# Optimization experiments

Hardware: AMD Instinct MI355X
Metric: run time of the kernel (lower is better)

Reference implementation:

```python
import jax, jax.numpy as jnp
import numpy as np

B, S, DIN, DH, NB = 4, 2048, 256, 128, 50
LN_EPS = 1e-5
THRESHOLDS = (0.5, 1.0, 2.0, 4.0)


def _layernorm(x, g, b):
    m = jnp.mean(x, axis=-1, keepdims=True)
    v = jnp.mean((x - m) ** 2, axis=-1, keepdims=True)
    return (x - m) * jax.lax.rsqrt(v + LN_EPS) * g + b


def setup_inputs() -> dict:
    key = jax.random.key(0)
    ks = jax.random.split(key, 12)
    single_repr = jax.random.normal(ks[0], (B, S, DIN), jnp.float32)
    # coordinates spread out so the <=15A local neighborhood is nontrivial
    coordinates = jax.random.normal(ks[1], (B, S, 3), jnp.float32) * 12.0
    mask = jnp.ones((B, S), jnp.float32)
    sc = 0.05
    return {
        'single_repr': single_repr,
        'coordinates': coordinates,
        'mask': mask,
        'W1': jax.random.normal(ks[2], (DIN, DH), jnp.float32) * sc,
        'b1': jnp.zeros((DH,), jnp.float32),
        'g1': jnp.ones((DH,), jnp.float32),
        'be1': jnp.zeros((DH,), jnp.float32),
        'W2': jax.random.normal(ks[3], (DH, DH), jnp.float32) * sc,
        'b2': jnp.zeros((DH,), jnp.float32),
        'g2': jnp.ones((DH,), jnp.float32),
        'be2': jnp.zeros((DH,), jnp.float32),
        'W3': jax.random.normal(ks[4], (DH, NB), jnp.float32) * sc,
        'b3': jnp.zeros((NB,), jnp.float32),
        'temperature': jnp.ones((1,), jnp.float32),
    }


def reference(single_repr, coordinates, mask, W1, b1, g1, be1, W2, b2, g2, be2, W3, b3, temperature):
    # ---- confidence MLP (dropout in eval mode = identity) ----
    h = jax.nn.relu(_layernorm(single_repr @ W1 + b1, g1, be1))
    h = jax.nn.relu(_layernorm(h @ W2 + b2, g2, be2))
    logits = (h @ W3 + b3) / temperature          # [B, S, NB]
    probs = jax.nn.softmax(logits, axis=-1)

    # ---- vectorized pLDDT (replaces the per-residue Python loop) ----
    diff = coordinates[:, :, None, :] - coordinates[:, None, :, :]   # [B,S,S,3]
    D = jnp.sqrt(jnp.sum(diff * diff, axis=-1))                      # [B,S,S]
    maskb = mask > 0.0
    local = (D <= 15.0) & maskb[:, :, None] & maskb[:, None, :]      # [B,S,S]
    counts = jnp.sum(local, axis=-1).astype(jnp.float32)             # [B,S]
    frac_sum = jnp.zeros((B, S), jnp.float32)
    for t in THRESHOLDS:  # fixed small loop over 4 thresholds
        within = jnp.sum((D <= t) & local, axis=-1).astype(jnp.float32)
        frac_sum = frac_sum + within / jnp.maximum(counts, 1.0)
    plddt = jnp.where(counts > 0, frac_sum / len(THRESHOLDS) * 100.0, 0.0)

    # ---- final masking, as in torch forward ----
    plddt = plddt * mask
    logits_m = logits * mask[:, :, None]
    probs_m = probs * mask[:, :, None]
    return plddt, logits_m, probs_m
```

## Files before the change

kernel.cpp:

```cpp
#include <hip/hip_runtime.h>
#include <float.h>
#include <math.h>

#define B_   4
#define S_   2048
#define DIN_ 256
#define DH_  128
#define NB_  50
#define NBP_ 64
#define ROWS (B_ * S_)
#define MB   16

#define MLP_BLOCKS   (ROWS / MB)
#define PLDDT_ROWSPB 32
#define PLDDT_BLOCKS (ROWS / PLDDT_ROWSPB)

typedef __attribute__((ext_vector_type(8))) short  short8;
typedef __attribute__((ext_vector_type(4))) float  f32x4;

__device__ __forceinline__ unsigned short bf16_rne(float f) {
    unsigned u = __builtin_bit_cast(unsigned, f);
    u = u + 0x7fffu + ((u >> 16) & 1u);
    return (unsigned short)(u >> 16);
}

__global__ __launch_bounds__(256) void setup_w(
    const float* __restrict__ W1, const float* __restrict__ W2,
    const float* __restrict__ W3, unsigned short* __restrict__ wt)
{
    const int t = blockIdx.x * 256 + threadIdx.x;
    const int l = t & 63, m = l & 15, kg = l >> 4;
    float src[8];
    int dst;
    if (t < 4096) {
        const int c = t >> 6, nt = c >> 3, ks = c & 7;
        const int n = nt * 16 + m, k = ks * 32 + kg * 8;
#pragma unroll
        for (int i = 0; i < 8; ++i) src[i] = W1[(k + i) * DH_ + n];
        dst = t * 8;
    } else if (t < 6144) {
        const int s = t - 4096, c = s >> 6, nt = c >> 2, ks = c & 3;
        const int n = nt * 16 + m, k = ks * 32 + kg * 8;
#pragma unroll
        for (int i = 0; i < 8; ++i) src[i] = W2[(k + i) * DH_ + n];
        dst = 32768 + s * 8;
    } else {
        const int s = t - 6144, c = s >> 6, nt = c >> 2, ks = c & 3;
        const int n = nt * 16 + m, k = ks * 32 + kg * 8;
#pragma unroll
        for (int i = 0; i < 8; ++i) src[i] = (n < NB_) ? W3[(k + i) * NB_ + n] : 0.f;
        dst = 49152 + s * 8;
    }
    union { short8 v; unsigned short u[8]; } H;
#pragma unroll
    for (int i = 0; i < 8; ++i) H.u[i] = bf16_rne(src[i]);
    *(short8*)&wt[dst] = H.v;
}

union SharedU {
    struct {
        unsigned short sA[MB * DIN_];
        float sStats[MB][20];
        float sL[MB * NBP_];
    } mlp;
    f32x4 sP[S_];
};

__global__ __launch_bounds__(512) void fused_kernel(
    const float* __restrict__ x, const float* __restrict__ coords,
    const float* __restrict__ mask,
    const float* __restrict__ b1, const float* __restrict__ g1, const float* __restrict__ be1,
    const float* __restrict__ b2, const float* __restrict__ g2, const float* __restrict__ be2,
    const float* __restrict__ b3, const float* __restrict__ temp,
    const unsigned short* __restrict__ wt,
    float* __restrict__ out_plddt,
    float* __restrict__ out_logits, float* __restrict__ out_probs)
{
    __shared__ SharedU sh;
    const int tid  = threadIdx.x;
    const int lane = tid & 63;
    const int w    = tid >> 6;

    if (blockIdx.x < MLP_BLOCKS) {
        unsigned short* sA = sh.mlp.sA;
        const int m    = lane & 15;
        const int kg   = lane >> 4;
        const int row0 = blockIdx.x * MB;

        {
            const int r  = tid >> 5;
            const int kc = (tid & 31) << 3;
            const float* xp = x + (size_t)(row0 + r) * DIN_ + kc;
            f32x4 a = *(const f32x4*)xp;
            f32x4 b = *(const f32x4*)(xp + 4);
            union { short8 v; unsigned short u[8]; } H;
#pragma unroll
            for (int i = 0; i < 8; ++i)
                H.u[i] = bf16_rne((i < 4) ? a[i] : b[i - 4]);
            const int idx = (r * 256 + kc) ^ ((r & 7) << 3);
            *(short8*)&sA[idx] = H.v;
        }
        __syncthreads();

        const int n12 = w * 16 + m;

        f32x4 aA = {0.f,0.f,0.f,0.f}, aB = {0.f,0.f,0.f,0.f};
        {
            const unsigned short* bp = wt + (w * 8) * 512;
#pragma unroll
            for (int ks = 0; ks < 8; ++ks) {
                const int ia = (m * 256 + ks * 32 + kg * 8) ^ ((m & 7) << 3);
                short8 ah = *(const short8*)&sA[ia];
                short8 bh = *(const short8*)&bp[ks * 512 + lane * 8];
                f32x4& ac = (ks & 1) ? aB : aA;
                ac = __builtin_amdgcn_mfma_f32_16x16x32_bf16(ah, bh, ac, 0, 0, 0);
            }
        }

        {
            const float bb = b1[n12], gg = g1[n12], ee = be1[n12];
            float v[4];
#pragma unroll
            for (int j = 0; j < 4; ++j) v[j] = aA[j] + aB[j] + bb;
#pragma unroll
            for (int j = 0; j < 4; ++j) {
                float sv = v[j], qv = v[j] * v[j];
                for (int off = 1; off < 16; off <<= 1) { sv += __shfl_xor(sv, off); qv += __shfl_xor(qv, off); }
                if (m == 0) { sh.mlp.sStats[kg * 4 + j][w * 2] = sv; sh.mlp.sStats[kg * 4 + j][w * 2 + 1] = qv; }
            }
            __syncthreads();
#pragma unroll
            for (int j = 0; j < 4; ++j) {
                const int r = kg * 4 + j;
                f32x4 s0 = *(const f32x4*)&sh.mlp.sStats[r][0];
                f32x4 s1 = *(const f32x4*)&sh.mlp.sStats[r][4];
                f32x4 s2 = *(const f32x4*)&sh.mlp.sStats[r][8];
                f32x4 s3 = *(const f32x4*)&sh.mlp.sStats[r][12];
                const float S = s0[0]+s0[2]+s1[0]+s1[2]+s2[0]+s2[2]+s3[0]+s3[2];
                const float Q = s0[1]+s0[3]+s1[1]+s1[3]+s2[1]+s2[3]+s3[1]+s3[3];
                const float mean = S * (1.f / DH_);
                const float inv  = rsqrtf(Q * (1.f / DH_) - mean * mean + 1e-5f);
                const float h = fmaxf(fmaf((v[j] - mean) * inv, gg, ee), 0.f);
                const int idx = (r * 128 + n12) ^ ((r & 7) << 3);
                sA[idx] = bf16_rne(h);
            }
        }
        __syncthreads();

        aA = (f32x4){0.f,0.f,0.f,0.f}; aB = (f32x4){0.f,0.f,0.f,0.f};
        {
            const unsigned short* bp = wt + 32768 + (w * 4) * 512;
#pragma unroll
            for (int ks = 0; ks < 4; ++ks) {
                const int ia = (m * 128 + ks * 32 + kg * 8) ^ ((m & 7) << 3);
                short8 ah = *(const short8*)&sA[ia];
                short8 bh = *(const short8*)&bp[ks * 512 + lane * 8];
                f32x4& ac = (ks & 1) ? aB : aA;
                ac = __builtin_amdgcn_mfma_f32_16x16x32_bf16(ah, bh, ac, 0, 0, 0);
            }
        }

        {
            const float bb = b2[n12], gg = g2[n12], ee = be2[n12];
            float v[4];
#pragma unroll
            for (int j = 0; j < 4; ++j) v[j] = aA[j] + aB[j] + bb;
#pragma unroll
            for (int j = 0; j < 4; ++j) {
                float sv = v[j], qv = v[j] * v[j];
                for (int off = 1; off < 16; off <<= 1) { sv += __shfl_xor(sv, off); qv += __shfl_xor(qv, off); }
                if (m == 0) { sh.mlp.sStats[kg * 4 + j][w * 2] = sv; sh.mlp.sStats[kg * 4 + j][w * 2 + 1] = qv; }
            }
            __syncthreads();
#pragma unroll
            for (int j = 0; j < 4; ++j) {
                const int r = kg * 4 + j;
                f32x4 s0 = *(const f32x4*)&sh.mlp.sStats[r][0];
                f32x4 s1 = *(const f32x4*)&sh.mlp.sStats[r][4];
                f32x4 s2 = *(const f32x4*)&sh.mlp.sStats[r][8];
                f32x4 s3 = *(const f32x4*)&sh.mlp.sStats[r][12];
                const float S = s0[0]+s0[2]+s1[0]+s1[2]+s2[0]+s2[2]+s3[0]+s3[2];
                const float Q = s0[1]+s0[3]+s1[1]+s1[3]+s2[1]+s2[3]+s3[1]+s3[3];
                const float mean = S * (1.f / DH_);
                const float inv  = rsqrtf(Q * (1.f / DH_) - mean * mean + 1e-5f);
                const float h = fmaxf(fmaf((v[j] - mean) * inv, gg, ee), 0.f);
                const int idx = (r * 128 + n12) ^ ((r & 7) << 3);
                sA[idx] = bf16_rne(h);
            }
        }
        __syncthreads();

        if (w < 4) {
            f32x4 cA = {0.f,0.f,0.f,0.f}, cB = {0.f,0.f,0.f,0.f};
            const unsigned short* bp = wt + 49152 + (w * 4) * 512;
#pragma unroll
            for (int ks = 0; ks < 4; ++ks) {
                const int ia = (m * 128 + ks * 32 + kg * 8) ^ ((m & 7) << 3);
                short8 ah = *(const short8*)&sA[ia];
                short8 bh = *(const short8*)&bp[ks * 512 + lane * 8];
                f32x4& ac = (ks & 1) ? cB : cA;
                ac = __builtin_amdgcn_mfma_f32_16x16x32_bf16(ah, bh, ac, 0, 0, 0);
            }
            const int n = w * 16 + m;
            const float bv = (n < NB_) ? b3[n] : 0.f;
            const float invT = 1.f / temp[0];
#pragma unroll
            for (int j = 0; j < 4; ++j)
                sh.mlp.sL[(kg * 4 + j) * NBP_ + n] = (cA[j] + cB[j] + bv) * invT;
        }
        __syncthreads();

        if (tid < 256) {
            const int r  = tid >> 4;
            const int c0 = (tid & 15) * 4;
            f32x4 lg = *(const f32x4*)&sh.mlp.sL[r * NBP_ + c0];
            float mx = -FLT_MAX;
#pragma unroll
            for (int i = 0; i < 4; ++i) if (c0 + i < NB_) mx = fmaxf(mx, lg[i]);
            for (int off = 1; off < 16; off <<= 1) mx = fmaxf(mx, __shfl_xor(mx, off));
            float e[4]; float sm = 0.f;
#pragma unroll
            for (int i = 0; i < 4; ++i) { e[i] = (c0 + i < NB_) ? expf(lg[i] - mx) : 0.f; sm += e[i]; }
            for (int off = 1; off < 16; off <<= 1) sm += __shfl_xor(sm, off);
            const float isum = 1.f / sm;
            const float mk = mask[row0 + r];
            float* ol = out_logits + (size_t)(row0 + r) * NB_;
            float* op = out_probs  + (size_t)(row0 + r) * NB_;
#pragma unroll
            for (int i = 0; i < 4; ++i) {
                const int c = c0 + i;
                if (c < NB_) { ol[c] = lg[i] * mk; op[c] = e[i] * isum * mk; }
            }
        }
    } else {
        const int pb   = blockIdx.x - MLP_BLOCKS;
        const int row0 = pb * PLDDT_ROWSPB;
        const int b    = row0 >> 11;
        const int ib0  = row0 & (S_ - 1);

        const float* cb = coords + (size_t)b * S_ * 3;
        const float* mb = mask   + (size_t)b * S_;

        {
            union { f32x4 v[3]; float f[12]; } C;
            const float* cp = cb + tid * 12;
#pragma unroll
            for (int q = 0; q < 3; ++q) C.v[q] = *(const f32x4*)(cp + q * 4);
            union { f32x4 v; float f[4]; } M;
            M.v = *(const f32x4*)(mb + tid * 4);
#pragma unroll
            for (int q = 0; q < 4; ++q)
                sh.sP[tid * 4 + q] = (f32x4){C.f[q*3], C.f[q*3+1], C.f[q*3+2], M.f[q]};
        }
        __syncthreads();

        f32x4 PI[4];
#pragma unroll
        for (int ii = 0; ii < 4; ++ii) PI[ii] = sh.sP[ib0 + w * 4 + ii];

        int cnt[4] = {0,0,0,0}, wsum[4] = {0,0,0,0};
        for (int j = lane; j < S_; j += 64) {
            const f32x4 p = sh.sP[j];
            const float gd = (p[3] > 0.f) ? 0.f : 1e30f;
#pragma unroll
            for (int ii = 0; ii < 4; ++ii) {
                const float dx = PI[ii][0] - p[0];
                const float dy = PI[ii][1] - p[1];
                const float dz = PI[ii][2] - p[2];
                const float d2 = fmaf(dx, dx, fmaf(dy, dy, dz * dz)) + gd;
                cnt[ii]  += (d2 <= 225.f);
                wsum[ii] += (d2 <= 16.f);
                wsum[ii] += (d2 <= 4.f);
                wsum[ii] += (d2 <= 1.f);
                wsum[ii] += (d2 <= 0.25f);
            }
        }
#pragma unroll
        for (int ii = 0; ii < 4; ++ii)
            for (int off = 32; off; off >>= 1) {
                cnt[ii]  += __shfl_xor(cnt[ii], off);
                wsum[ii] += __shfl_xor(wsum[ii], off);
            }
        if (lane == 0) {
#pragma unroll
            for (int ii = 0; ii < 4; ++ii) {
                const float fc = (float)cnt[ii];
                const float r  = (cnt[ii] > 0) ? (wsum[ii] * 25.f / fc) : 0.f;
                out_plddt[row0 + w * 4 + ii] = r * PI[ii][3];
            }
        }
    }
}

extern "C" void kernel_launch(void* const* d_in, const int* in_sizes, int n_in,
                              void* d_out, int out_size, void* d_ws, size_t ws_size,
                              hipStream_t stream) {
    const float* x      = (const float*)d_in[0];
    const float* coords = (const float*)d_in[1];
    const float* mask   = (const float*)d_in[2];
    const float* W1  = (const float*)d_in[3];
    const float* b1  = (const float*)d_in[4];
    const float* g1  = (const float*)d_in[5];
    const float* be1 = (const float*)d_in[6];
    const float* W2  = (const float*)d_in[7];
    const float* b2  = (const float*)d_in[8];
    const float* g2  = (const float*)d_in[9];
    const float* be2 = (const float*)d_in[10];
    const float* W3  = (const float*)d_in[11];
    const float* b3  = (const float*)d_in[12];
    const float* temp= (const float*)d_in[13];

    float* out        = (float*)d_out;
    float* out_plddt  = out;
    float* out_logits = out + (size_t)ROWS;
    float* out_probs  = out_logits + (size_t)ROWS * NB_;

    unsigned short* wt = (unsigned short*)d_ws;

    setup_w<<<28, 256, 0, stream>>>(W1, W2, W3, wt);
    fused_kernel<<<MLP_BLOCKS + PLDDT_BLOCKS, 512, 0, stream>>>(
        x, coords, mask, b1, g1, be1, b2, g2, be2, b3, temp, wt,
        out_plddt, out_logits, out_probs);
}
```

Before: 25.50 us.

## Give each wave full 16-row MLP tile to drop block-level syncs and LDS stats

After: 43.47 us. 1.7x slower.

```diff
diff --git a/kernel.cpp b/kernel.cpp
--- a/kernel.cpp
+++ b/kernel.cpp
@@ -7,13 +7,12 @@
 #define DIN_ 256
 #define DH_  128
 #define NB_  50
-#define NBP_ 64
 #define ROWS (B_ * S_)
-#define MB   16
-
-#define MLP_BLOCKS   (ROWS / MB)
-#define PLDDT_ROWSPB 32
-#define PLDDT_BLOCKS (ROWS / PLDDT_ROWSPB)
+
+#define MB_ROWS 64
+#define MLP_BLOCKS (ROWS / MB_ROWS)
+#define PL_ROWS 16
+#define PL_BLOCKS (ROWS / PL_ROWS)
 
 typedef __attribute__((ext_vector_type(8))) short  short8;
 typedef __attribute__((ext_vector_type(4))) float  f32x4;
@@ -57,16 +56,7 @@
     *(short8*)&wt[dst] = H.v;
 }
 
-union SharedU {
-    struct {
-        unsigned short sA[MB * DIN_];
-        float sStats[MB][20];
-        float sL[MB * NBP_];
-    } mlp;
-    f32x4 sP[S_];
-};
-
-__global__ __launch_bounds__(512) void fused_kernel(
+__global__ __launch_bounds__(256) void fused_kernel(
     const float* __restrict__ x, const float* __restrict__ coords,
     const float* __restrict__ mask,
     const float* __restrict__ b1, const float* __restrict__ g1, const float* __restrict__ be1,
@@ -76,165 +66,200 @@
     float* __restrict__ out_plddt,
     float* __restrict__ out_logits, float* __restrict__ out_probs)
 {
-    __shared__ SharedU sh;
+    __shared__ union { unsigned short sX[MB_ROWS * DIN_]; f32x4 sP[S_]; } sh;
     const int tid  = threadIdx.x;
     const int lane = tid & 63;
     const int w    = tid >> 6;
 
     if (blockIdx.x < MLP_BLOCKS) {
-        unsigned short* sA = sh.mlp.sA;
-        const int m    = lane & 15;
-        const int kg   = lane >> 4;
-        const int row0 = blockIdx.x * MB;
+        const int row0 = blockIdx.x * MB_ROWS;
+        const int m  = lane & 15;
+        const int kg = lane >> 4;
+
+#pragma unroll
+        for (int q = 0; q < 8; ++q) {
+            const int idx = q * 2048 + tid * 8;
+            const float* xp = x + (size_t)row0 * DIN_ + idx;
+            f32x4 va = *(const f32x4*)xp;
+            f32x4 vb = *(const f32x4*)(xp + 4);
+            union { short8 v; unsigned short u[8]; } H;
+#pragma unroll
+            for (int i = 0; i < 8; ++i)
+                H.u[i] = bf16_rne((i < 4) ? va[i] : vb[i - 4]);
+            const int r = idx >> 8, c = idx & 255;
+            *(short8*)&sh.sX[(r * 256 + c) ^ ((r & 7) << 3)] = H.v;
+        }
+        __syncthreads();
+
+        const int wb = w * 4096;
+
+        short8 a1[8];
+#pragma unroll
+        for (int ks = 0; ks < 8; ++ks)
+            a1[ks] = *(const short8*)&sh.sX[wb + ((m * 256 + ks * 32 + kg * 8) ^ ((m & 7) << 3))];
+        f32x4 acc[8];
+#pragma unroll
+        for (int nt = 0; nt < 8; ++nt) acc[nt] = (f32x4){0.f, 0.f, 0.f, 0.f};
+#pragma unroll
+        for (int nt = 0; nt < 8; ++nt)
+#pragma unroll
+            for (int ks = 0; ks < 8; ++ks) {
+                short8 bh = *(const short8*)&wt[(nt * 8 + ks) * 512 + lane * 8];
+                acc[nt] = __builtin_amdgcn_mfma_f32_16x16x32_bf16(a1[ks], bh, acc[nt], 0, 0, 0);
+            }
 
         {
-            const int r  = tid >> 5;
-            const int kc = (tid & 31) << 3;
-            const float* xp = x + (size_t)(row0 + r) * DIN_ + kc;
-            f32x4 a = *(const f32x4*)xp;
-            f32x4 b = *(const f32x4*)(xp + 4);
-            union { short8 v; unsigned short u[8]; } H;
-#pragma unroll
-            for (int i = 0; i < 8; ++i)
-                H.u[i] = bf16_rne((i < 4) ? a[i] : b[i - 4]);
-            const int idx = (r * 256 + kc) ^ ((r & 7) << 3);
-            *(short8*)&sA[idx] = H.v;
-        }
-        __syncthreads();
-
-        const int n12 = w * 16 + m;
-
-        f32x4 aA = {0.f,0.f,0.f,0.f}, aB = {0.f,0.f,0.f,0.f};
+            float v[8][4], Sj[4] = {0,0,0,0}, Qj[4] = {0,0,0,0};
+#pragma unroll
+            for (int nt = 0; nt < 8; ++nt) {
+                const float bv = b1[nt * 16 + m];
+#pragma unroll
+                for (int j = 0; j < 4; ++j) {
+                    const float t = acc[nt][j] + bv;
+                    v[nt][j] = t; Sj[j] += t; Qj[j] += t * t;
+                }
+            }
+#pragma unroll
+            for (int j = 0; j < 4; ++j)
+                for (int off = 1; off < 16; off <<= 1) {
+                    Sj[j] += __shfl_xor(Sj[j], off);
+                    Qj[j] += __shfl_xor(Qj[j], off);
+                }
+            float mean[4], inv[4];
+#pragma unroll
+            for (int j = 0; j < 4; ++j) {
+                mean[j] = Sj[j] * (1.f / DH_);
+                inv[j]  = rsqrtf(Qj[j] * (1.f / DH_) - mean[j] * mean[j] + 1e-5f);
+            }
+#pragma unroll
+            for (int nt = 0; nt < 8; ++nt) {
+                const float gv = g1[nt * 16 + m], ev = be1[nt * 16 + m];
+#pragma unroll
+                for (int j = 0; j < 4; ++j) {
+                    const float h = fmaxf(fmaf((v[nt][j] - mean[j]) * inv[j], gv, ev), 0.f);
+                    const int r = kg * 4 + j;
+                    sh.sX[wb + ((r * 128 + nt * 16 + m) ^ ((r & 7) << 3))] = bf16_rne(h);
+                }
+            }
+        }
+
+        short8 a2[4];
+#pragma unroll
+        for (int ks = 0; ks < 4; ++ks)
+            a2[ks] = *(const short8*)&sh.sX[wb + ((m * 128 + ks * 32 + kg * 8) ^ ((m & 7) << 3))];
+        f32x4 acc2[8];
+#pragma unroll
+        for (int nt = 0; nt < 8; ++nt) acc2[nt] = (f32x4){0.f, 0.f, 0.f, 0.f};
+#pragma unroll
+        for (int nt = 0; nt < 8; ++nt)
+#pragma unroll
+            for (int ks = 0; ks < 4; ++ks) {
+                short8 bh = *(const short8*)&wt[32768 + (nt * 4 + ks) * 512 + lane * 8];
+                acc2[nt] = __builtin_amdgcn_mfma_f32_16x16x32_bf16(a2[ks], bh, acc2[nt], 0, 0, 0);
+            }
+
         {
-            const unsigned short* bp = wt + (w * 8) * 512;
-#pragma unroll
-            for (int ks = 0; ks < 8; ++ks) {
-                const int ia = (m * 256 + ks * 32 + kg * 8) ^ ((m & 7) << 3);
-                short8 ah = *(const short8*)&sA[ia];
-                short8 bh = *(const short8*)&bp[ks * 512 + lane * 8];
-                f32x4& ac = (ks & 1) ? aB : aA;
-                ac = __builtin_amdgcn_mfma_f32_16x16x32_bf16(ah, bh, ac, 0, 0, 0);
+            float v[8][4], Sj[4] = {0,0,0,0}, Qj[4] = {0,0,0,0};
+#pragma unroll
+            for (int nt = 0; nt < 8; ++nt) {
+                const float bv = b2[nt * 16 + m];
+#pragma unroll
+                for (int j = 0; j < 4; ++j) {
+                    const float t = acc2[nt][j] + bv;
+                    v[nt][j] = t; Sj[j] += t; Qj[j] += t * t;
+                }
+            }
+#pragma unroll
+            for (int j = 0; j < 4; ++j)
+                for (int off = 1; off < 16; off <<= 1) {
+                    Sj[j] += __shfl_xor(Sj[j], off);
+                    Qj[j] += __shfl_xor(Qj[j], off);
+                }
+            float mean[4], inv[4];
+#pragma unroll
+            for (int j = 0; j < 4; ++j) {
+                mean[j] = Sj[j] * (1.f / DH_);
+                inv[j]  = rsqrtf(Qj[j] * (1.f / DH_) - mean[j] * mean[j] + 1e-5f);
+            }
+#pragma unroll
+            for (int nt = 0; nt < 8; ++nt) {
+                const float gv = g2[nt * 16 + m], ev = be2[nt * 16 + m];
+#pragma unroll
+                for (int j = 0; j < 4; ++j) {
+                    const float h = fmaxf(fmaf((v[nt][j] - mean[j]) * inv[j], gv, ev), 0.f);
+                    const int r = kg * 4 + j;
+                    sh.sX[wb + ((r * 128 + nt * 16 + m) ^ ((r & 7) << 3))] = bf16_rne(h);
+                }
             }
         }
 
         {
-            const float bb = b1[n12], gg = g1[n12], ee = be1[n12];
-            float v[4];
-#pragma unroll
-            for (int j = 0; j < 4; ++j) v[j] = aA[j] + aB[j] + bb;
+            short8 a3[4];
+#pragma unroll
+            for (int ks = 0; ks < 4; ++ks)
+                a3[ks] = *(const short8*)&sh.sX[wb + ((m * 128 + ks * 32 + kg * 8) ^ ((m & 7) << 3))];
+            f32x4 acc3[4];
+#pragma unroll
+            for (int nt = 0; nt < 4; ++nt) acc3[nt] = (f32x4){0.f, 0.f, 0.f, 0.f};
+#pragma unroll
+            for (int nt = 0; nt < 4; ++nt)
+#pragma unroll
+                for (int ks = 0; ks < 4; ++ks) {
+                    short8 bh = *(const short8*)&wt[49152 + (nt * 4 + ks) * 512 + lane * 8];
+                    acc3[nt] = __builtin_amdgcn_mfma_f32_16x16x32_bf16(a3[ks], bh, acc3[nt], 0, 0, 0);
+                }
+            const float invT = 1.f / temp[0];
+            float lv[4][4], ev[4][4], mx[4], sm[4];
+#pragma unroll
+            for (int j = 0; j < 4; ++j) { mx[j] = -FLT_MAX; sm[j] = 0.f; }
+#pragma unroll
+            for (int nt = 0; nt < 4; ++nt) {
+                const int col = nt * 16 + m;
+                const float bv = (col < NB_) ? b3[col] : 0.f;
+#pragma unroll
+                for (int j = 0; j < 4; ++j) {
+                    const float t = (acc3[nt][j] + bv) * invT;
+                    lv[nt][j] = t;
+                    if (col < NB_) mx[j] = fmaxf(mx[j], t);
+                }
+            }
+#pragma unroll
+            for (int j = 0; j < 4; ++j)
+                for (int off = 1; off < 16; off <<= 1)
+                    mx[j] = fmaxf(mx[j], __shfl_xor(mx[j], off));
+#pragma unroll
+            for (int nt = 0; nt < 4; ++nt) {
+                const int col = nt * 16 + m;
+#pragma unroll
+                for (int j = 0; j < 4; ++j) {
+                    const float e = (col < NB_) ? expf(lv[nt][j] - mx[j]) : 0.f;
+                    ev[nt][j] = e; sm[j] += e;
+                }
+            }
+#pragma unroll
+            for (int j = 0; j < 4; ++j)
+                for (int off = 1; off < 16; off <<= 1)
+                    sm[j] += __shfl_xor(sm[j], off);
 #pragma unroll
             for (int j = 0; j < 4; ++j) {
-                float sv = v[j], qv = v[j] * v[j];
-                for (int off = 1; off < 16; off <<= 1) { sv += __shfl_xor(sv, off); qv += __shfl_xor(qv, off); }
-                if (m == 0) { sh.mlp.sStats[kg * 4 + j][w * 2] = sv; sh.mlp.sStats[kg * 4 + j][w * 2 + 1] = qv; }
-            }
-            __syncthreads();
-#pragma unroll
-            for (int j = 0; j < 4; ++j) {
-                const int r = kg * 4 + j;
-                f32x4 s0 = *(const f32x4*)&sh.mlp.sStats[r][0];
-                f32x4 s1 = *(const f32x4*)&sh.mlp.sStats[r][4];
-                f32x4 s2 = *(const f32x4*)&sh.mlp.sStats[r][8];
-                f32x4 s3 = *(const f32x4*)&sh.mlp.sStats[r][12];
-                const float S = s0[0]+s0[2]+s1[0]+s1[2]+s2[0]+s2[2]+s3[0]+s3[2];
-                const float Q = s0[1]+s0[3]+s1[1]+s1[3]+s2[1]+s2[3]+s3[1]+s3[3];
-                const float mean = S * (1.f / DH_);
-                const float inv  = rsqrtf(Q * (1.f / DH_) - mean * mean + 1e-5f);
-                const float h = fmaxf(fmaf((v[j] - mean) * inv, gg, ee), 0.f);
-                const int idx = (r * 128 + n12) ^ ((r & 7) << 3);
-                sA[idx] = bf16_rne(h);
-            }
-        }
-        __syncthreads();
-
-        aA = (f32x4){0.f,0.f,0.f,0.f}; aB = (f32x4){0.f,0.f,0.f,0.f};
-        {
-            const unsigned short* bp = wt + 32768 + (w * 4) * 512;
-#pragma unroll
-            for (int ks = 0; ks < 4; ++ks) {
-                const int ia = (m * 128 + ks * 32 + kg * 8) ^ ((m & 7) << 3);
-                short8 ah = *(const short8*)&sA[ia];
-                short8 bh = *(const short8*)&bp[ks * 512 + lane * 8];
-                f32x4& ac = (ks & 1) ? aB : aA;
-                ac = __builtin_amdgcn_mfma_f32_16x16x32_bf16(ah, bh, ac, 0, 0, 0);
-            }
-        }
-
-        {
-            const float bb = b2[n12], gg = g2[n12], ee = be2[n12];
-            float v[4];
-#pragma unroll
-            for (int j = 0; j < 4; ++j) v[j] = aA[j] + aB[j] + bb;
-#pragma unroll
-            for (int j = 0; j < 4; ++j) {
-                float sv = v[j], qv = v[j] * v[j];
-                for (int off = 1; off < 16; off <<= 1) { sv += __shfl_xor(sv, off); qv += __shfl_xor(qv, off); }
-                if (m == 0) { sh.mlp.sStats[kg * 4 + j][w * 2] = sv; sh.mlp.sStats[kg * 4 + j][w * 2 + 1] = qv; }
-            }
-            __syncthreads();
-#pragma unroll
-            for (int j = 0; j < 4; ++j) {
-                const int r = kg * 4 + j;
-                f32x4 s0 = *(const f32x4*)&sh.mlp.sStats[r][0];
-                f32x4 s1 = *(const f32x4*)&sh.mlp.sStats[r][4];
-                f32x4 s2 = *(const f32x4*)&sh.mlp.sStats[r][8];
-                f32x4 s3 = *(const f32x4*)&sh.mlp.sStats[r][12];
-                const float S = s0[0]+s0[2]+s1[0]+s1[2]+s2[0]+s2[2]+s3[0]+s3[2];
-                const float Q = s0[1]+s0[3]+s1[1]+s1[3]+s2[1]+s2[3]+s3[1]+s3[3];
-                const float mean = S * (1.f / DH_);
-                const float inv  = rsqrtf(Q * (1.f / DH_) - mean * mean + 1e-5f);
-                const float h = fmaxf(fmaf((v[j] - mean) * inv, gg, ee), 0.f);
-                const int idx = (r * 128 + n12) ^ ((r & 7) << 3);
-                sA[idx] = bf16_rne(h);
-            }
-        }
-        __syncthreads();
-
-        if (w < 4) {
-            f32x4 cA = {0.f,0.f,0.f,0.f}, cB = {0.f,0.f,0.f,0.f};
-            const unsigned short* bp = wt + 49152 + (w * 4) * 512;
-#pragma unroll
-            for (int ks = 0; ks < 4; ++ks) {
-                const int ia = (m * 128 + ks * 32 + kg * 8) ^ ((m & 7) << 3);
-                short8 ah = *(const short8*)&sA[ia];
-                short8 bh = *(const short8*)&bp[ks * 512 + lane * 8];
-                f32x4& ac = (ks & 1) ? cB : cA;
-                ac = __builtin_amdgcn_mfma_f32_16x16x32_bf16(ah, bh, ac, 0, 0, 0);
-            }
-            const int n = w * 16 + m;
-            const float bv = (n < NB_) ? b3[n] : 0.f;
-            const float invT = 1.f / temp[0];
-#pragma unroll
-            for (int j = 0; j < 4; ++j)
-                sh.mlp.sL[(kg * 4 + j) * NBP_ + n] = (cA[j] + cB[j] + bv) * invT;
-        }
-        __syncthreads();
-
-        if (tid < 256) {
-            const int r  = tid >> 4;
-            const int c0 = (tid & 15) * 4;
-            f32x4 lg = *(const f32x4*)&sh.mlp.sL[r * NBP_ + c0];
-            float mx = -FLT_MAX;
-#pragma unroll
-            for (int i = 0; i < 4; ++i) if (c0 + i < NB_) mx = fmaxf(mx, lg[i]);
-            for (int off = 1; off < 16; off <<= 1) mx = fmaxf(mx, __shfl_xor(mx, off));
-            float e[4]; float sm = 0.f;
-#pragma unroll
-            for (int i = 0; i < 4; ++i) { e[i] = (c0 + i < NB_) ? expf(lg[i] - mx) : 0.f; sm += e[i]; }
-            for (int off = 1; off < 16; off <<= 1) sm += __shfl_xor(sm, off);
-            const float isum = 1.f / sm;
-            const float mk = mask[row0 + r];
-            float* ol = out_logits + (size_t)(row0 + r) * NB_;
-            float* op = out_probs  + (size_t)(row0 + r) * NB_;
-#pragma unroll
-            for (int i = 0; i < 4; ++i) {
-                const int c = c0 + i;
-                if (c < NB_) { ol[c] = lg[i] * mk; op[c] = e[i] * isum * mk; }
+                const float isum = 1.f / sm[j];
+                const int ra = row0 + w * 16 + kg * 4 + j;
+                const float mk = mask[ra];
+                float* ol = out_logits + (size_t)ra * NB_;
+                float* op = out_probs  + (size_t)ra * NB_;
+#pragma unroll
+                for (int nt = 0; nt < 4; ++nt) {
+                    const int col = nt * 16 + m;
+                    if (col < NB_) {
+                        ol[col] = lv[nt][j] * mk;
+                        op[col] = ev[nt][j] * isum * mk;
+                    }
+                }
             }
         }
     } else {
         const int pb   = blockIdx.x - MLP_BLOCKS;
-        const int row0 = pb * PLDDT_ROWSPB;
+        const int row0 = pb * PL_ROWS;
         const int b    = row0 >> 11;
         const int ib0  = row0 & (S_ - 1);
 
@@ -242,15 +267,16 @@
         const float* mb = mask   + (size_t)b * S_;
 
         {
-            union { f32x4 v[3]; float f[12]; } C;
-            const float* cp = cb + tid * 12;
-#pragma unroll
-            for (int q = 0; q < 3; ++q) C.v[q] = *(const f32x4*)(cp + q * 4);
-            union { f32x4 v; float f[4]; } M;
-            M.v = *(const f32x4*)(mb + tid * 4);
-#pragma unroll
-            for (int q = 0; q < 4; ++q)
-                sh.sP[tid * 4 + q] = (f32x4){C.f[q*3], C.f[q*3+1], C.f[q*3+2], M.f[q]};
+            union { f32x4 v[6]; float f[24]; } C;
+            const float* cp = cb + tid * 24;
+#pragma unroll
+            for (int q = 0; q < 6; ++q) C.v[q] = *(const f32x4*)(cp + q * 4);
+            union { f32x4 v[2]; float f[8]; } M;
+            M.v[0] = *(const f32x4*)(mb + tid * 8);
+            M.v[1] = *(const f32x4*)(mb + tid * 8 + 4);
+#pragma unroll
+            for (int q = 0; q < 8; ++q)
+                sh.sP[tid * 8 + q] = (f32x4){C.f[q*3], C.f[q*3+1], C.f[q*3+2], M.f[q]};
         }
         __syncthreads();
 
@@ -318,7 +344,7 @@
     unsigned short* wt = (unsigned short*)d_ws;
 
     setup_w<<<28, 256, 0, stream>>>(W1, W2, W3, wt);
-    fused_kernel<<<MLP_BLOCKS + PLDDT_BLOCKS, 512, 0, stream>>>(
+    fused_kernel<<<MLP_BLOCKS + PL_BLOCKS, 256, 0, stream>>>(
         x, coords, mask, b1, g1, be1, b2, g2, be2, b3, temp, wt,
         out_plddt, out_logits, out_probs);
 }
```

## Process 32 rows per MLP block and reuse weight fragments held in registers

Applied to the files above, without the earlier changes.

Result: no change. 25.65 us (+0.6%).

```diff
diff --git a/kernel.cpp b/kernel.cpp
--- a/kernel.cpp
+++ b/kernel.cpp
@@ -9,7 +9,7 @@
 #define NB_  50
 #define NBP_ 64
 #define ROWS (B_ * S_)
-#define MB   16
+#define MB   32
 
 #define MLP_BLOCKS   (ROWS / MB)
 #define PLDDT_ROWSPB 32
@@ -87,130 +87,172 @@
         const int kg   = lane >> 4;
         const int row0 = blockIdx.x * MB;
 
-        {
-            const int r  = tid >> 5;
-            const int kc = (tid & 31) << 3;
-            const float* xp = x + (size_t)(row0 + r) * DIN_ + kc;
-            f32x4 a = *(const f32x4*)xp;
-            f32x4 b = *(const f32x4*)(xp + 4);
+        short8 pb1[8];
+#pragma unroll
+        for (int ks = 0; ks < 8; ++ks)
+            pb1[ks] = *(const short8*)&wt[(w * 8 + ks) * 512 + lane * 8];
+
+#pragma unroll
+        for (int q = 0; q < 2; ++q) {
+            const int idx = q * 4096 + tid * 8;
+            const float* xp = x + (size_t)row0 * DIN_ + idx;
+            f32x4 va = *(const f32x4*)xp;
+            f32x4 vb = *(const f32x4*)(xp + 4);
             union { short8 v; unsigned short u[8]; } H;
 #pragma unroll
             for (int i = 0; i < 8; ++i)
-                H.u[i] = bf16_rne((i < 4) ? a[i] : b[i - 4]);
-            const int idx = (r * 256 + kc) ^ ((r & 7) << 3);
-            *(short8*)&sA[idx] = H.v;
+                H.u[i] = bf16_rne((i < 4) ? va[i] : vb[i - 4]);
+            const int r = idx >> 8, c = idx & 255;
+            *(short8*)&sA[(r * 256 + c) ^ ((r & 7) << 3)] = H.v;
         }
         __syncthreads();
 
         const int n12 = w * 16 + m;
 
-        f32x4 aA = {0.f,0.f,0.f,0.f}, aB = {0.f,0.f,0.f,0.f};
-        {
-            const unsigned short* bp = wt + (w * 8) * 512;
-#pragma unroll
-            for (int ks = 0; ks < 8; ++ks) {
-                const int ia = (m * 256 + ks * 32 + kg * 8) ^ ((m & 7) << 3);
-                short8 ah = *(const short8*)&sA[ia];
-                short8 bh = *(const short8*)&bp[ks * 512 + lane * 8];
-                f32x4& ac = (ks & 1) ? aB : aA;
-                ac = __builtin_amdgcn_mfma_f32_16x16x32_bf16(ah, bh, ac, 0, 0, 0);
-            }
-        }
+        f32x4 aA = {0,0,0,0}, aB = {0,0,0,0}, aC = {0,0,0,0}, aD = {0,0,0,0};
+#pragma unroll
+        for (int ks = 0; ks < 8; ++ks) {
+            const int ia = (m * 256 + ks * 32 + kg * 8) ^ ((m & 7) << 3);
+            short8 a0 = *(const short8*)&sA[ia];
+            short8 a1v = *(const short8*)&sA[ia + 16 * 256];
+            f32x4& t0 = (ks & 1) ? aB : aA;
+            f32x4& t1 = (ks & 1) ? aD : aC;
+            t0 = __builtin_amdgcn_mfma_f32_16x16x32_bf16(a0,  pb1[ks], t0, 0, 0, 0);
+            t1 = __builtin_amdgcn_mfma_f32_16x16x32_bf16(a1v, pb1[ks], t1, 0, 0, 0);
+        }
+
+        short8 pb2[4];
+#pragma unroll
+        for (int ks = 0; ks < 4; ++ks)
+            pb2[ks] = *(const short8*)&wt[32768 + (w * 4 + ks) * 512 + lane * 8];
 
         {
             const float bb = b1[n12], gg = g1[n12], ee = be1[n12];
-            float v[4];
-#pragma unroll
-            for (int j = 0; j < 4; ++j) v[j] = aA[j] + aB[j] + bb;
+            float v0[4], v1[4];
 #pragma unroll
             for (int j = 0; j < 4; ++j) {
-                float sv = v[j], qv = v[j] * v[j];
-                for (int off = 1; off < 16; off <<= 1) { sv += __shfl_xor(sv, off); qv += __shfl_xor(qv, off); }
-                if (m == 0) { sh.mlp.sStats[kg * 4 + j][w * 2] = sv; sh.mlp.sStats[kg * 4 + j][w * 2 + 1] = qv; }
+                v0[j] = aA[j] + aB[j] + bb;
+                v1[j] = aC[j] + aD[j] + bb;
+            }
+#pragma unroll
+            for (int j = 0; j < 4; ++j) {
+                float s0 = v0[j], q0 = v0[j] * v0[j];
+                float s1 = v1[j], q1 = v1[j] * v1[j];
+                for (int off = 1; off < 16; off <<= 1) {
+                    s0 += __shfl_xor(s0, off); q0 += __shfl_xor(q0, off);
+                    s1 += __shfl_xor(s1, off); q1 += __shfl_xor(q1, off);
+                }
+                if (m == 0) {
+                    const int r = kg * 4 + j;
+                    sh.mlp.sStats[r][w * 2] = s0;      sh.mlp.sStats[r][w * 2 + 1] = q0;
+                    sh.mlp.sStats[r + 16][w * 2] = s1; sh.mlp.sStats[r + 16][w * 2 + 1] = q1;
+                }
             }
             __syncthreads();
 #pragma unroll
+            for (int t = 0; t < 2; ++t) {
+#pragma unroll
+                for (int j = 0; j < 4; ++j) {
+                    const int r = t * 16 + kg * 4 + j;
+                    f32x4 s0 = *(const f32x4*)&sh.mlp.sStats[r][0];
+                    f32x4 s1 = *(const f32x4*)&sh.mlp.sStats[r][4];
+                    f32x4 s2 = *(const f32x4*)&sh.mlp.sStats[r][8];
+                    f32x4 s3 = *(const f32x4*)&sh.mlp.sStats[r][12];
+                    const float S = s0[0]+s0[2]+s1[0]+s1[2]+s2[0]+s2[2]+s3[0]+s3[2];
+                    const float Q = s0[1]+s0[3]+s1[1]+s1[3]+s2[1]+s2[3]+s3[1]+s3[3];
+                    const float mean = S * (1.f / DH_);
+                    const float inv  = rsqrtf(Q * (1.f / DH_) - mean * mean + 1e-5f);
+                    const float vv = t ? (aC[j] + aD[j] + bb) : (aA[j] + aB[j] + bb);
+                    const float h = fmaxf(fmaf((vv - mean) * inv, gg, ee), 0.f);
+                    sA[(r * 128 + n12) ^ ((r & 7) << 3)] = bf16_rne(h);
+                }
+            }
+        }
+        __syncthreads();
+
+        aA = (f32x4){0,0,0,0}; aB = (f32x4){0,0,0,0};
+        aC = (f32x4){0,0,0,0}; aD = (f32x4){0,0,0,0};
+#pragma unroll
+        for (int ks = 0; ks < 4; ++ks) {
+            const int ia = (m * 128 + ks * 32 + kg * 8) ^ ((m & 7) << 3);
+            short8 a0 = *(const short8*)&sA[ia];
+            short8 a1v = *(const short8*)&sA[ia + 16 * 128];
+            f32x4& t0 = (ks & 1) ? aB : aA;
+            f32x4& t1 = (ks & 1) ? aD : aC;
+            t0 = __builtin_amdgcn_mfma_f32_16x16x32_bf16(a0,  pb2[ks], t0, 0, 0, 0);
+            t1 = __builtin_amdgcn_mfma_f32_16x16x32_bf16(a1v, pb2[ks], t1, 0, 0, 0);
+        }
+
+        short8 pb3[4];
+#pragma unroll
+        for (int ks = 0; ks < 4; ++ks)
+            pb3[ks] = *(const short8*)&wt[49152 + ((w & 3) * 4 + ks) * 512 + lane * 8];
+
+        {
+            const float bb = b2[n12], gg = g2[n12], ee = be2[n12];
+            float v0[4], v1[4];
+#pragma unroll
             for (int j = 0; j < 4; ++j) {
-                const int r = kg * 4 + j;
-                f32x4 s0 = *(const f32x4*)&sh.mlp.sStats[r][0];
-                f32x4 s1 = *(const f32x4*)&sh.mlp.sStats[r][4];
-                f32x4 s2 = *(const f32x4*)&sh.mlp.sStats[r][8];
-                f32x4 s3 = *(const f32x4*)&sh.mlp.sStats[r][12];
-                const float S = s0[0]+s0[2]+s1[0]+s1[2]+s2[0]+s2[2]+s3[0]+s3[2];
-                const float Q = s0[1]+s0[3]+s1[1]+s1[3]+s2[1]+s2[3]+s3[1]+s3[3];
-                const float mean = S * (1.f / DH_);
-                const float inv  = rsqrtf(Q * (1.f / DH_) - mean * mean + 1e-5f);
-                const float h = fmaxf(fmaf((v[j] - mean) * inv, gg, ee), 0.f);
-                const int idx = (r * 128 + n12) ^ ((r & 7) << 3);
-                sA[idx] = bf16_rne(h);
-            }
-        }
-        __syncthreads();
-
-        aA = (f32x4){0.f,0.f,0.f,0.f}; aB = (f32x4){0.f,0.f,0.f,0.f};
-        {
-            const unsigned short* bp = wt + 32768 + (w * 4) * 512;
+                v0[j] = aA[j] + aB[j] + bb;
+                v1[j] = aC[j] + aD[j] + bb;
+            }
+#pragma unroll
+            for (int j = 0; j < 4; ++j) {
+                float s0 = v0[j], q0 = v0[j] * v0[j];
+                float s1 = v1[j], q1 = v1[j] * v1[j];
+                for (int off = 1; off < 16; off <<= 1) {
+                    s0 += __shfl_xor(s0, off); q0 += __shfl_xor(q0, off);
+                    s1 += __shfl_xor(s1, off); q1 += __shfl_xor(q1, off);
+                }
+                if (m == 0) {
+                    const int r = kg * 4 + j;
+                    sh.mlp.sStats[r][w * 2] = s0;      sh.mlp.sStats[r][w * 2 + 1] = q0;
+                    sh.mlp.sStats[r + 16][w * 2] = s1; sh.mlp.sStats[r + 16][w * 2 + 1] = q1;
+                }
+            }
+            __syncthreads();
+#pragma unroll
+            for (int t = 0; t < 2; ++t) {
+#pragma unroll
+                for (int j = 0; j < 4; ++j) {
+                    const int r = t * 16 + kg * 4 + j;
+                    f32x4 s0 = *(const f32x4*)&sh.mlp.sStats[r][0];
+                    f32x4 s1 = *(const f32x4*)&sh.mlp.sStats[r][4];
+                    f32x4 s2 = *(const f32x4*)&sh.mlp.sStats[r][8];
+                    f32x4 s3 = *(const f32x4*)&sh.mlp.sStats[r][12];
+                    const float S = s0[0]+s0[2]+s1[0]+s1[2]+s2[0]+s2[2]+s3[0]+s3[2];
+                    const float Q = s0[1]+s0[3]+s1[1]+s1[3]+s2[1]+s2[3]+s3[1]+s3[3];
+                    const float mean = S * (1.f / DH_);
+                    const float inv  = rsqrtf(Q * (1.f / DH_) - mean * mean + 1e-5f);
+                    const float vv = t ? (aC[j] + aD[j] + bb) : (aA[j] + aB[j] + bb);
+                    const float h = fmaxf(fmaf((vv - mean) * inv, gg, ee), 0.f);
+                    sA[(r * 128 + n12) ^ ((r & 7) << 3)] = bf16_rne(h);
+                }
+            }
+        }
+        __syncthreads();
+
+        {
+            const int ti = w >> 2;
+            const int ng = w & 3;
+            f32x4 cA = {0,0,0,0}, cB = {0,0,0,0};
 #pragma unroll
             for (int ks = 0; ks < 4; ++ks) {
-                const int ia = (m * 128 + ks * 32 + kg * 8) ^ ((m & 7) << 3);
-                short8 ah = *(const short8*)&sA[ia];
-                short8 bh = *(const short8*)&bp[ks * 512 + lane * 8];
-                f32x4& ac = (ks & 1) ? aB : aA;
-                ac = __builtin_amdgcn_mfma_f32_16x16x32_bf16(ah, bh, ac, 0, 0, 0);
-            }
-        }
-
-        {
-            const float bb = b2[n12], gg = g2[n12], ee = be2[n12];
-            float v[4];
-#pragma unroll
-            for (int j = 0; j < 4; ++j) v[j] = aA[j] + aB[j] + bb;
-#pragma unroll
-            for (int j = 0; j < 4; ++j) {
-                float sv = v[j], qv = v[j] * v[j];
-                for (int off = 1; off < 16; off <<= 1) { sv += __shfl_xor(sv, off); qv += __shfl_xor(qv, off); }
-                if (m == 0) { sh.mlp.sStats[kg * 4 + j][w * 2] = sv; sh.mlp.sStats[kg * 4 + j][w * 2 + 1] = qv; }
-            }
-            __syncthreads();
-#pragma unroll
-            for (int j = 0; j < 4; ++j) {
-                const int r = kg * 4 + j;
-                f32x4 s0 = *(const f32x4*)&sh.mlp.sStats[r][0];
-                f32x4 s1 = *(const f32x4*)&sh.mlp.sStats[r][4];
-                f32x4 s2 = *(const f32x4*)&sh.mlp.sStats[r][8];
-                f32x4 s3 = *(const f32x4*)&sh.mlp.sStats[r][12];
-                const float S = s0[0]+s0[2]+s1[0]+s1[2]+s2[0]+s2[2]+s3[0]+s3[2];
-                const float Q = s0[1]+s0[3]+s1[1]+s1[3]+s2[1]+s2[3]+s3[1]+s3[3];
-                const float mean = S * (1.f / DH_);
-                const float inv  = rsqrtf(Q * (1.f / DH_) - mean * mean + 1e-5f);
-                const float h = fmaxf(fmaf((v[j] - mean) * inv, gg, ee), 0.f);
-                const int idx = (r * 128 + n12) ^ ((r & 7) << 3);
-                sA[idx] = bf16_rne(h);
-            }
-        }
-        __syncthreads();
-
-        if (w < 4) {
-            f32x4 cA = {0.f,0.f,0.f,0.f}, cB = {0.f,0.f,0.f,0.f};
-            const unsigned short* bp = wt + 49152 + (w * 4) * 512;
-#pragma unroll
-            for (int ks = 0; ks < 4; ++ks) {
-                const int ia = (m * 128 + ks * 32 + kg * 8) ^ ((m & 7) << 3);
-                short8 ah = *(const short8*)&sA[ia];
-                short8 bh = *(const short8*)&bp[ks * 512 + lane * 8];
+                const int ia = ((m * 128 + ks * 32 + kg * 8) ^ ((m & 7) << 3)) + ti * 2048;
+                short8 a0 = *(const short8*)&sA[ia];
                 f32x4& ac = (ks & 1) ? cB : cA;
-                ac = __builtin_amdgcn_mfma_f32_16x16x32_bf16(ah, bh, ac, 0, 0, 0);
-            }
-            const int n = w * 16 + m;
-            const float bv = (n < NB_) ? b3[n] : 0.f;
+                ac = __builtin_amdgcn_mfma_f32_16x16x32_bf16(a0, pb3[ks], ac, 0, 0, 0);
+            }
+            const int col = ng * 16 + m;
+            const float bv = (col < NB_) ? b3[col] : 0.f;
             const float invT = 1.f / temp[0];
 #pragma unroll
             for (int j = 0; j < 4; ++j)
-                sh.mlp.sL[(kg * 4 + j) * NBP_ + n] = (cA[j] + cB[j] + bv) * invT;
-        }
-        __syncthreads();
-
-        if (tid < 256) {
+                sh.mlp.sL[(ti * 16 + kg * 4 + j) * NBP_ + col] = (cA[j] + cB[j] + bv) * invT;
+        }
+        __syncthreads();
+
+        {
             const int r  = tid >> 4;
             const int c0 = (tid & 15) * 4;
             f32x4 lg = *(const f32x4*)&sh.mlp.sL[r * NBP_ + c0];
```
